# Performance work log

Hardware: AMD Instinct MI355X
Metric: run time of the kernel (lower is better)

The kernel has to match this reference:

```python
import jax, jax.numpy as jnp
import numpy as np

B, S, D = 8, 1024, 1024
H, DH = 16, 64  # n_heads, d_head; D == H*DH


def setup_inputs() -> dict:
    key = jax.random.key(0)
    ks = jax.random.split(key, 7)
    scale = 1.0 / np.sqrt(DH)
    return {
        "images": jax.random.normal(ks[0], (B, S, D), dtype=jnp.float32),
        "Wq": jax.random.normal(ks[1], (H, DH, DH), dtype=jnp.float32) * scale,
        "bq": jax.random.normal(ks[2], (H, DH), dtype=jnp.float32) * scale,
        "Wk": jax.random.normal(ks[3], (H, DH, DH), dtype=jnp.float32) * scale,
        "bk": jax.random.normal(ks[4], (H, DH), dtype=jnp.float32) * scale,
        "Wv": jax.random.normal(ks[5], (H, DH, DH), dtype=jnp.float32) * scale,
        "bv": jax.random.normal(ks[6], (H, DH), dtype=jnp.float32) * scale,
    }


def reference(images, Wq, bq, Wk, bk, Wv, bv):
    Bn, Sn, Dn = images.shape
    x = images.reshape(Bn, Sn, H, DH)  # split hidden dim into per-head slices
    # torch Linear: y = x @ W.T + b, per head -> einsum over input dim d
    q = jnp.einsum("bshd,hod->bsho", x, Wq) + bq  # [B,S,H,DH]
    k = jnp.einsum("bshd,hod->bsho", x, Wk) + bk
    v = jnp.einsum("bshd,hod->bsho", x, Wv) + bv
    scores = jnp.einsum("bqhd,bkhd->bhqk", q, k) / jnp.sqrt(jnp.asarray(DH, x.dtype))
    attn = jax.nn.softmax(scores, axis=-1)  # [B,H,S,S]
    out = jnp.einsum("bhqk,bkhd->bqhd", attn, v)  # [B,S,H,DH]
    return out.reshape(Bn, Sn, Dn)  # hstack across heads == reshape back
```

## Files before the change

### kernel.cpp

```cpp
#include <hip/hip_runtime.h>
#include <hip/hip_bf16.h>

#define B_ 8
#define S_ 1024
#define D_ 1024
#define H_ 16
#define DH_ 64

typedef __attribute__((ext_vector_type(8))) short short8;
typedef __attribute__((ext_vector_type(8))) unsigned short ushort8;
typedef __attribute__((ext_vector_type(4))) unsigned short us4;
typedef __attribute__((ext_vector_type(4))) unsigned int uint4v;
typedef __attribute__((ext_vector_type(4))) float f32x4;

#define QSCALE 0.18033688011112042f

static __device__ __forceinline__ unsigned short f2bf(float f) {
    union { float f; unsigned u; } v; v.f = f;
    unsigned r = v.u + 0x7fffu + ((v.u >> 16) & 1u);
    return (unsigned short)(r >> 16);
}

static __device__ __forceinline__ void stage8(const float* __restrict__ src, unsigned short* dst) {
    float4 a = *reinterpret_cast<const float4*>(src);
    float4 b = *reinterpret_cast<const float4*>(src + 4);
    ushort8 r;
    r[0] = f2bf(a.x); r[1] = f2bf(a.y); r[2] = f2bf(a.z); r[3] = f2bf(a.w);
    r[4] = f2bf(b.x); r[5] = f2bf(b.y); r[6] = f2bf(b.z); r[7] = f2bf(b.w);
    *reinterpret_cast<ushort8*>(dst) = r;
}

static __device__ __forceinline__ unsigned int cvtpk(float a, float b) {
    unsigned int r;
    asm("v_cvt_pk_bf16_f32 %0, %1, %2" : "=v"(r) : "v"(a), "v"(b));
    return r;
}

static __device__ __forceinline__ void gll16(const void* g, void* l) {
    __builtin_amdgcn_global_load_lds(
        (const __attribute__((address_space(1))) unsigned int*)g,
        (__attribute__((address_space(3))) unsigned int*)l,
        16, 0, 0);
}

__global__ __launch_bounds__(256) void qkv_proj(
    const float* __restrict__ x,
    const float* __restrict__ Wq, const float* __restrict__ bq,
    const float* __restrict__ Wk, const float* __restrict__ bk,
    const float* __restrict__ Wv, const float* __restrict__ bv,
    unsigned short* __restrict__ qo, unsigned short* __restrict__ ko,
    unsigned short* __restrict__ vo)
{
    const int bid   = blockIdx.x;
    const int stile = bid & 15;
    const int h     = (bid >> 4) & (H_ - 1);
    const int b     = bid >> 8;
    const int tid   = threadIdx.x;
    const int lane  = tid & 63;
    const int wave  = tid >> 6;
    const int lr    = lane & 15;
    const int lk    = lane >> 4;

    __shared__ __align__(16) unsigned short xs[64][72];
    __shared__ __align__(16) unsigned short wsh[3][64][72];

    {
        int row = tid >> 2;
        int col = (tid & 3) * 16;
        const float* src = x + ((size_t)(b * S_ + stile * 64 + row)) * D_ + h * DH_ + col;
        stage8(src,     &xs[row][col]);
        stage8(src + 8, &xs[row][col + 8]);
        const float* wsrc[3] = { Wq + h * DH_ * DH_, Wk + h * DH_ * DH_, Wv + h * DH_ * DH_ };
        #pragma unroll
        for (int p = 0; p < 3; ++p) {
            const float* s = wsrc[p] + row * DH_ + col;
            stage8(s,     &wsh[p][row][col]);
            stage8(s + 8, &wsh[p][row][col + 8]);
        }
    }
    __syncthreads();

    short8 a[2];
    #pragma unroll
    for (int kk = 0; kk < 2; ++kk)
        a[kk] = *reinterpret_cast<const short8*>(&xs[wave * 16 + lr][8 * lk + 32 * kk]);

    f32x4 acc[3][4];
    #pragma unroll
    for (int p = 0; p < 3; ++p)
        #pragma unroll
        for (int n = 0; n < 4; ++n)
            acc[p][n] = (f32x4){0.f, 0.f, 0.f, 0.f};

    #pragma unroll
    for (int p = 0; p < 3; ++p)
        #pragma unroll
        for (int kk = 0; kk < 2; ++kk)
            #pragma unroll
            for (int n = 0; n < 4; ++n) {
                short8 bf = *reinterpret_cast<const short8*>(&wsh[p][lr + 16 * n][8 * lk + 32 * kk]);
                acc[p][n] = __builtin_amdgcn_mfma_f32_16x16x32_bf16(a[kk], bf, acc[p][n], 0, 0, 0);
            }

    size_t base = ((size_t)(b * H_ + h) * S_ + stile * 64 + wave * 16) * DH_;
    #pragma unroll
    for (int p = 0; p < 2; ++p) {
        const float* bias = p ? (bk + h * DH_) : (bq + h * DH_);
        unsigned short* op = p ? ko : qo;
        #pragma unroll
        for (int n = 0; n < 4; ++n) {
            int col = lr + 16 * n;
            float bb = bias[col];
            #pragma unroll
            for (int r = 0; r < 4; ++r) {
                float val = acc[p][n][r] + bb;
                if (p == 0) val *= QSCALE;
                op[base + (size_t)(4 * lk + r) * DH_ + col] = f2bf(val);
            }
        }
    }
    {
        size_t vbase = (size_t)(b * H_ + h) * DH_ * S_;
        int s0 = stile * 64 + wave * 16 + 4 * lk;
        #pragma unroll
        for (int n = 0; n < 4; ++n) {
            int dh = lr + 16 * n;
            float bb = bv[h * DH_ + dh];
            us4 w;
            #pragma unroll
            for (int r = 0; r < 4; ++r) w[r] = f2bf(acc[2][n][r] + bb);
            *reinterpret_cast<us4*>(vo + vbase + (size_t)dh * S_ + s0) = w;
        }
    }
}

__global__ __launch_bounds__(256, 2) void attn_fwd(
    const unsigned short* __restrict__ q,
    const unsigned short* __restrict__ k,
    const unsigned short* __restrict__ vt,
    float* __restrict__ out)
{
    const int bid   = (blockIdx.x & 7) * 64 + (blockIdx.x >> 3);
    const int qtile = bid & 3;
    const int h     = (bid >> 2) & (H_ - 1);
    const int b     = bid >> 6;
    const int tid   = threadIdx.x;
    const int lane  = tid & 63;
    const int wave  = tid >> 6;
    const int lr    = lane & 15;
    const int lk    = lane >> 4;

    __shared__ __align__(16) unsigned short ks[2][64][64];
    __shared__ __align__(16) unsigned short vs[2][64][64];

    const size_t bh = (size_t)(b * H_ + h) * S_ * DH_;

    short8 qf[4][2];
    #pragma unroll
    for (int g = 0; g < 4; ++g) {
        const unsigned short* qp = q + bh + (size_t)(qtile * 256 + wave * 64 + 16 * g + lr) * DH_;
        #pragma unroll
        for (int kk = 0; kk < 2; ++kk)
            qf[g][kk] = *reinterpret_cast<const short8*>(qp + 8 * lk + 32 * kk);
    }

    const int rp0 = 16 * wave + (lane >> 3);
    const int rp1 = rp0 + 8;
    const int c   = lane & 7;
    const int gk0 = (rp0 & 0x23) | ((rp0 & 0x10) >> 2) | ((rp0 & 0x0C) << 1);
    const int gk1 = (rp1 & 0x23) | ((rp1 & 0x10) >> 2) | ((rp1 & 0x0C) << 1);
    const size_t kofs0 = (size_t)gk0 * DH_ + (c ^ (rp0 & 7)) * 8;
    const size_t kofs1 = (size_t)gk1 * DH_ + (c ^ (rp1 & 7)) * 8;
    const size_t vofs0 = (size_t)rp0 * S_ + (c ^ (rp0 & 7)) * 8;
    const size_t vofs1 = (size_t)rp1 * S_ + (c ^ (rp1 & 7)) * 8;
    const unsigned short* kb = k + bh;
    const unsigned short* vb = vt + bh;

    gll16(kb + kofs0, &ks[0][16 * wave][0]);
    gll16(kb + kofs1, &ks[0][16 * wave + 8][0]);
    gll16(vb + vofs0, &vs[0][16 * wave][0]);
    gll16(vb + vofs1, &vs[0][16 * wave + 8][0]);

    f32x4 acc[4][4];
    #pragma unroll
    for (int g = 0; g < 4; ++g)
        #pragma unroll
        for (int n = 0; n < 4; ++n) acc[g][n] = (f32x4){0.f, 0.f, 0.f, 0.f};
    float l[4] = {0.f, 0.f, 0.f, 0.f};

    const int rx = lr & 7;
    const int NT = S_ / 64;
    for (int t = 0; t < NT; ++t) {
        __syncthreads();
        const int cur = t & 1;

        if (t + 1 < NT) {
            const int nxt = cur ^ 1;
            const unsigned short* kt = kb + (size_t)(t + 1) * 64 * DH_;
            const unsigned short* vtb = vb + (size_t)(t + 1) * 64;
            gll16(kt + kofs0, &ks[nxt][16 * wave][0]);
            gll16(kt + kofs1, &ks[nxt][16 * wave + 8][0]);
            gll16(vtb + vofs0, &vs[nxt][16 * wave][0]);
            gll16(vtb + vofs1, &vs[nxt][16 * wave + 8][0]);
        }

        f32x4 st[4][4];
        #pragma unroll
        for (int g = 0; g < 4; ++g)
            #pragma unroll
            for (int n = 0; n < 4; ++n) st[g][n] = (f32x4){0.f, 0.f, 0.f, 0.f};
        #pragma unroll
        for (int kk = 0; kk < 2; ++kk)
            #pragma unroll
            for (int n = 0; n < 4; ++n) {
                short8 ka = *reinterpret_cast<const short8*>(
                    &ks[cur][16 * n + lr][((lk + 4 * kk) ^ rx) * 8]);
                #pragma unroll
                for (int g = 0; g < 4; ++g)
                    st[g][n] = __builtin_amdgcn_mfma_f32_16x16x32_bf16(ka, qf[g][kk], st[g][n], 0, 0, 0);
            }

        #pragma unroll
        for (int g = 0; g < 4; ++g) {
            #pragma unroll
            for (int n = 0; n < 4; ++n)
                #pragma unroll
                for (int r = 0; r < 4; ++r)
                    st[g][n][r] = __builtin_amdgcn_exp2f(st[g][n][r]);
            float a0 = (st[g][0][0] + st[g][0][1]) + (st[g][0][2] + st[g][0][3]);
            float a1 = (st[g][1][0] + st[g][1][1]) + (st[g][1][2] + st[g][1][3]);
            float a2 = (st[g][2][0] + st[g][2][1]) + (st[g][2][2] + st[g][2][3]);
            float a3 = (st[g][3][0] + st[g][3][1]) + (st[g][3][2] + st[g][3][3]);
            l[g] += (a0 + a1) + (a2 + a3);
        }

        short8 pa[4][2];
        #pragma unroll
        for (int g = 0; g < 4; ++g)
            #pragma unroll
            for (int kk = 0; kk < 2; ++kk) {
                uint4v w4;
                w4[0] = cvtpk(st[g][2 * kk][0],     st[g][2 * kk][1]);
                w4[1] = cvtpk(st[g][2 * kk][2],     st[g][2 * kk][3]);
                w4[2] = cvtpk(st[g][2 * kk + 1][0], st[g][2 * kk + 1][1]);
                w4[3] = cvtpk(st[g][2 * kk + 1][2], st[g][2 * kk + 1][3]);
                pa[g][kk] = __builtin_bit_cast(short8, w4);
            }

        #pragma unroll
        for (int kk = 0; kk < 2; ++kk)
            #pragma unroll
            for (int n = 0; n < 4; ++n) {
                short8 va = *reinterpret_cast<const short8*>(
                    &vs[cur][16 * n + lr][((lk + 4 * kk) ^ rx) * 8]);
                #pragma unroll
                for (int g = 0; g < 4; ++g)
                    acc[g][n] = __builtin_amdgcn_mfma_f32_16x16x32_bf16(va, pa[g][kk], acc[g][n], 0, 0, 0);
            }
    }

    #pragma unroll
    for (int g = 0; g < 4; ++g) {
        float lg = l[g];
        lg += __shfl_xor(lg, 16, 64);
        lg += __shfl_xor(lg, 32, 64);
        const float inv = 1.f / lg;
        const int qrow = qtile * 256 + wave * 64 + 16 * g + lr;
        float* op = out + (size_t)(b * S_ + qrow) * D_ + h * DH_;
        #pragma unroll
        for (int n = 0; n < 4; ++n) {
            float4 o;
            o.x = acc[g][n][0] * inv; o.y = acc[g][n][1] * inv;
            o.z = acc[g][n][2] * inv; o.w = acc[g][n][3] * inv;
            *reinterpret_cast<float4*>(op + 16 * n + 4 * lk) = o;
        }
    }
}

extern "C" void kernel_launch(void* const* d_in, const int* in_sizes, int n_in,
                              void* d_out, int out_size, void* d_ws, size_t ws_size,
                              hipStream_t stream) {
    const float* x  = (const float*)d_in[0];
    const float* Wq = (const float*)d_in[1];
    const float* bq = (const float*)d_in[2];
    const float* Wk = (const float*)d_in[3];
    const float* bk = (const float*)d_in[4];
    const float* Wv = (const float*)d_in[5];
    const float* bv = (const float*)d_in[6];
    float* out = (float*)d_out;

    unsigned short* qw = (unsigned short*)d_ws;
    size_t per = (size_t)B_ * H_ * S_ * DH_;
    unsigned short* kw = qw + per;
    unsigned short* vw = kw + per;

    qkv_proj<<<dim3(B_ * H_ * (S_ / 64)), 256, 0, stream>>>(x, Wq, bq, Wk, bk, Wv, bv, qw, kw, vw);
    attn_fwd<<<dim3(B_ * H_ * (S_ / 256)), 256, 0, stream>>>(qw, kw, vw, out);
}
```

Baseline: 66.60 us.

## Triple-buffer K/V tiles and interleave per-group QK/softmax/PV with priority hints

Moves K/V shared-memory staging from double to triple buffering, prefetching two tiles ahead. Each iteration ends with an explicit vmcnt wait plus a raw barrier instead of __syncthreads. All K and V fragments are loaded from LDS up front, and the loop is reordered so each row group g runs QK MFMA, exp2 and PV MFMA in sequence, wrapped in s_setprio to favour matrix issue. The aim is to hide global-load latency and overlap softmax VALU work with MFMA, at the cost of more LDS, which may reduce occupancy, and higher register pressure.

```diff
diff --git a/kernel.cpp b/kernel.cpp
--- a/kernel.cpp
+++ b/kernel.cpp
@@ -150,8 +150,8 @@
     const int lr    = lane & 15;
     const int lk    = lane >> 4;
 
-    __shared__ __align__(16) unsigned short ks[2][64][64];
-    __shared__ __align__(16) unsigned short vs[2][64][64];
+    __shared__ __align__(16) unsigned short ks[3][64][64];
+    __shared__ __align__(16) unsigned short vs[3][64][64];
 
     const size_t bh = (size_t)(b * H_ + h) * S_ * DH_;
 
@@ -180,6 +180,18 @@
     gll16(kb + kofs1, &ks[0][16 * wave + 8][0]);
     gll16(vb + vofs0, &vs[0][16 * wave][0]);
     gll16(vb + vofs1, &vs[0][16 * wave + 8][0]);
+    {
+        const unsigned short* kt = kb + (size_t)64 * DH_;
+        const unsigned short* vtb = vb + 64;
+        gll16(kt + kofs0, &ks[1][16 * wave][0]);
+        gll16(kt + kofs1, &ks[1][16 * wave + 8][0]);
+        gll16(vtb + vofs0, &vs[1][16 * wave][0]);
+        gll16(vtb + vofs1, &vs[1][16 * wave + 8][0]);
+    }
+    asm volatile("s_waitcnt vmcnt(4)" ::: "memory");
+    __builtin_amdgcn_sched_barrier(0);
+    __builtin_amdgcn_s_barrier();
+    __builtin_amdgcn_sched_barrier(0);
 
     f32x4 acc[4][4];
     #pragma unroll
@@ -191,72 +203,78 @@
     const int rx = lr & 7;
     const int NT = S_ / 64;
     for (int t = 0; t < NT; ++t) {
-        __syncthreads();
-        const int cur = t & 1;
-
-        if (t + 1 < NT) {
-            const int nxt = cur ^ 1;
-            const unsigned short* kt = kb + (size_t)(t + 1) * 64 * DH_;
-            const unsigned short* vtb = vb + (size_t)(t + 1) * 64;
-            gll16(kt + kofs0, &ks[nxt][16 * wave][0]);
-            gll16(kt + kofs1, &ks[nxt][16 * wave + 8][0]);
-            gll16(vtb + vofs0, &vs[nxt][16 * wave][0]);
-            gll16(vtb + vofs1, &vs[nxt][16 * wave + 8][0]);
-        }
-
-        f32x4 st[4][4];
-        #pragma unroll
-        for (int g = 0; g < 4; ++g)
-            #pragma unroll
-            for (int n = 0; n < 4; ++n) st[g][n] = (f32x4){0.f, 0.f, 0.f, 0.f};
-        #pragma unroll
-        for (int kk = 0; kk < 2; ++kk)
-            #pragma unroll
-            for (int n = 0; n < 4; ++n) {
-                short8 ka = *reinterpret_cast<const short8*>(
-                    &ks[cur][16 * n + lr][((lk + 4 * kk) ^ rx) * 8]);
+        const int bc = t % 3;
+
+        if (t + 2 < NT) {
+            const int bn = (t + 2) % 3;
+            const unsigned short* kt = kb + (size_t)(t + 2) * 64 * DH_;
+            const unsigned short* vtb = vb + (size_t)(t + 2) * 64;
+            gll16(kt + kofs0, &ks[bn][16 * wave][0]);
+            gll16(kt + kofs1, &ks[bn][16 * wave + 8][0]);
+            gll16(vtb + vofs0, &vs[bn][16 * wave][0]);
+            gll16(vtb + vofs1, &vs[bn][16 * wave + 8][0]);
+        }
+
+        short8 ka[8], va[8];
+        #pragma unroll
+        for (int i = 0; i < 8; ++i) {
+            const int kk = i >> 2, n = i & 3;
+            const int col = ((lk + 4 * kk) ^ rx) * 8;
+            ka[i] = *reinterpret_cast<const short8*>(&ks[bc][16 * n + lr][col]);
+            va[i] = *reinterpret_cast<const short8*>(&vs[bc][16 * n + lr][col]);
+        }
+
+        #pragma unroll
+        for (int g = 0; g < 4; ++g) {
+            f32x4 st[4];
+            #pragma unroll
+            for (int n = 0; n < 4; ++n) st[n] = (f32x4){0.f, 0.f, 0.f, 0.f};
+            __builtin_amdgcn_s_setprio(1);
+            #pragma unroll
+            for (int kk = 0; kk < 2; ++kk)
                 #pragma unroll
-                for (int g = 0; g < 4; ++g)
-                    st[g][n] = __builtin_amdgcn_mfma_f32_16x16x32_bf16(ka, qf[g][kk], st[g][n], 0, 0, 0);
-            }
-
-        #pragma unroll
-        for (int g = 0; g < 4; ++g) {
+                for (int n = 0; n < 4; ++n)
+                    st[n] = __builtin_amdgcn_mfma_f32_16x16x32_bf16(ka[4 * kk + n], qf[g][kk], st[n], 0, 0, 0);
+            __builtin_amdgcn_s_setprio(0);
+
             #pragma unroll
             for (int n = 0; n < 4; ++n)
                 #pragma unroll
                 for (int r = 0; r < 4; ++r)
-                    st[g][n][r] = __builtin_amdgcn_exp2f(st[g][n][r]);
-            float a0 = (st[g][0][0] + st[g][0][1]) + (st[g][0][2] + st[g][0][3]);
-            float a1 = (st[g][1][0] + st[g][1][1]) + (st[g][1][2] + st[g][1][3]);
-            float a2 = (st[g][2][0] + st[g][2][1]) + (st[g][2][2] + st[g][2][3]);
-            float a3 = (st[g][3][0] + st[g][3][1]) + (st[g][3][2] + st[g][3][3]);
+                    st[n][r] = __builtin_amdgcn_exp2f(st[n][r]);
+            float a0 = (st[0][0] + st[0][1]) + (st[0][2] + st[0][3]);
+            float a1 = (st[1][0] + st[1][1]) + (st[1][2] + st[1][3]);
+            float a2 = (st[2][0] + st[2][1]) + (st[2][2] + st[2][3]);
+            float a3 = (st[3][0] + st[3][1]) + (st[3][2] + st[3][3]);
             l[g] += (a0 + a1) + (a2 + a3);
-        }
-
-        short8 pa[4][2];
-        #pragma unroll
-        for (int g = 0; g < 4; ++g)
+
+            short8 pa[2];
             #pragma unroll
             for (int kk = 0; kk < 2; ++kk) {
                 uint4v w4;
-                w4[0] = cvtpk(st[g][2 * kk][0],     st[g][2 * kk][1]);
-                w4[1] = cvtpk(st[g][2 * kk][2],     st[g][2 * kk][3]);
-                w4[2] = cvtpk(st[g][2 * kk + 1][0], st[g][2 * kk + 1][1]);
-                w4[3] = cvtpk(st[g][2 * kk + 1][2], st[g][2 * kk + 1][3]);
-                pa[g][kk] = __builtin_bit_cast(short8, w4);
+                w4[0] = cvtpk(st[2 * kk][0],     st[2 * kk][1]);
+                w4[1] = cvtpk(st[2 * kk][2],     st[2 * kk][3]);
+                w4[2] = cvtpk(st[2 * kk + 1][0], st[2 * kk + 1][1]);
+                w4[3] = cvtpk(st[2 * kk + 1][2], st[2 * kk + 1][3]);
+                pa[kk] = __builtin_bit_cast(short8, w4);
             }
 
-        #pragma unroll
-        for (int kk = 0; kk < 2; ++kk)
-            #pragma unroll
-            for (int n = 0; n < 4; ++n) {
-                short8 va = *reinterpret_cast<const short8*>(
-                    &vs[cur][16 * n + lr][((lk + 4 * kk) ^ rx) * 8]);
+            __builtin_amdgcn_s_setprio(1);
+            #pragma unroll
+            for (int kk = 0; kk < 2; ++kk)
                 #pragma unroll
-                for (int g = 0; g < 4; ++g)
-                    acc[g][n] = __builtin_amdgcn_mfma_f32_16x16x32_bf16(va, pa[g][kk], acc[g][n], 0, 0, 0);
-            }
+                for (int n = 0; n < 4; ++n)
+                    acc[g][n] = __builtin_amdgcn_mfma_f32_16x16x32_bf16(va[4 * kk + n], pa[kk], acc[g][n], 0, 0, 0);
+            __builtin_amdgcn_s_setprio(0);
+        }
+
+        if (t + 1 < NT) {
+            if (t + 2 < NT) asm volatile("s_waitcnt vmcnt(4)" ::: "memory");
+            else            asm volatile("s_waitcnt vmcnt(0)" ::: "memory");
+            __builtin_amdgcn_sched_barrier(0);
+            __builtin_amdgcn_s_barrier();
+            __builtin_amdgcn_sched_barrier(0);
+        }
     }
 
     #pragma unroll
```

Result: no change. 65.68 us (-1.4%).
